# Kernel tuning notes

Hardware: AMD Instinct MI355X
Metric: run time of the kernel (lower is better)

## Reference

```python
import jax, jax.numpy as jnp
import numpy as np

N_NODES = 100000
N_EDGES = 600000
D = 128  # input_dim == output_dim (required by index_add into zeros_like(x) + residual)
EPS = 1e-5


def _linear_params(key, d_in, d_out):
    kw, kb = jax.random.split(key)
    bound = 1.0 / np.sqrt(d_in)
    w = jax.random.uniform(kw, (d_in, d_out), minval=-bound, maxval=bound, dtype=jnp.float32)
    b = jax.random.uniform(kb, (d_out,), minval=-bound, maxval=bound, dtype=jnp.float32)
    return w, b


def setup_inputs() -> dict:
    key = jax.random.key(0)
    ks = jax.random.split(key, 6)
    x = jax.random.normal(ks[0], (N_NODES, D), dtype=jnp.float32)
    edge_index = jax.random.randint(ks[1], (2, N_EDGES), 0, N_NODES, dtype=jnp.int32)
    w_m1, b_m1 = _linear_params(ks[2], 2 * D, D)
    w_m2, b_m2 = _linear_params(ks[3], D, D)
    w_u1, b_u1 = _linear_params(ks[4], 2 * D, D)
    w_u2, b_u2 = _linear_params(ks[5], D, D)
    gamma = jnp.ones((D,), dtype=jnp.float32)
    beta = jnp.zeros((D,), dtype=jnp.float32)
    return {
        "x": x, "edge_index": edge_index,
        "w_m1": w_m1, "b_m1": b_m1, "w_m2": w_m2, "b_m2": b_m2,
        "w_u1": w_u1, "b_u1": b_u1, "w_u2": w_u2, "b_u2": b_u2,
        "gamma": gamma, "beta": beta,
    }


def _layernorm(h, gamma, beta):
    mu = jnp.mean(h, axis=-1, keepdims=True)
    var = jnp.mean(jnp.square(h - mu), axis=-1, keepdims=True)
    return (h - mu) * jax.lax.rsqrt(var + EPS) * gamma + beta


def reference(x, edge_index, w_m1, b_m1, w_m2, b_m2, w_u1, b_u1, w_u2, b_u2, gamma, beta):
    row, col = edge_index[0], edge_index[1]
    # message MLP on concat of gathered endpoints: [E, 2D] -> [E, D]
    m_in = jnp.concatenate([x[row], x[col]], axis=-1)
    m = jax.nn.relu(m_in @ w_m1 + b_m1) @ w_m2 + b_m2
    # scatter-add messages to destination nodes (index_add along dim 0 with col)
    agg = jax.ops.segment_sum(m, col, num_segments=x.shape[0])
    # update MLP on [N, 2D] -> [N, D]
    u_in = jnp.concatenate([x, agg], axis=-1)
    h = jax.nn.relu(u_in @ w_u1 + b_u1) @ w_u2 + b_u2
    return _layernorm(h, gamma, beta) + x
```

## Files before the change

kernel.cpp:

```cpp
#include <hip/hip_runtime.h>
#include <hip/hip_bf16.h>
#include <stdint.h>

#define N_NODES 100000
#define N_EDGES 600000
#define D 128
#define EPS 1e-5f
#define SCAN_BS 512
#define ROW_MASK 0x1FFFF

#define PREP_BLOCKS 321
#define HIST_BLOCKS 2344
#define XF_BLOCKS   3125
#define SC_BLOCKS   2344
#define AGG_BLOCKS  12500
#define UPD_BLOCKS  3125

typedef __attribute__((ext_vector_type(8))) short short8;
typedef __attribute__((ext_vector_type(16))) float floatx16;


__device__ __forceinline__ uint32_t pack_bf16_rne(float lo, float hi) {
    uint32_t ul = __builtin_bit_cast(uint32_t, lo);
    uint32_t uh = __builtin_bit_cast(uint32_t, hi);
    ul += 0x7fffu + ((ul >> 16) & 1u);
    uh += 0x7fffu + ((uh >> 16) & 1u);
    return (ul >> 16) | (uh & 0xffff0000u);
}

__device__ __forceinline__ unsigned short f32_to_bf16_rne(float f) {
    uint32_t u = __builtin_bit_cast(uint32_t, f);
    u += 0x7fffu + ((u >> 16) & 1u);
    return (unsigned short)(u >> 16);
}

__device__ __forceinline__ float bflo(uint32_t a) { return __builtin_bit_cast(float, a << 16); }
__device__ __forceinline__ float bfhi(uint32_t a) { return __builtin_bit_cast(float, a & 0xffff0000u); }

__global__ void prep_hist(const float* __restrict__ w_m1, const float* __restrict__ w_u1,
                          const float* __restrict__ w_u2, const float* __restrict__ w_m2,
                          const float* __restrict__ b_m2,
                          unsigned short* __restrict__ wm1f, unsigned short* __restrict__ wu1tf,
                          unsigned short* __restrict__ wu2f, unsigned short* __restrict__ wcf,
                          float* __restrict__ vb,
                          const int* __restrict__ col, int* __restrict__ count,
                          int* __restrict__ rank) {
    if (blockIdx.x >= PREP_BLOCKS) {
        int e = (blockIdx.x - PREP_BLOCKS) * 256 + threadIdx.x;
        if (e < N_EDGES) rank[e] = atomicAdd(&count[col[e]], 1);
        return;
    }
    int idx = blockIdx.x * 256 + threadIdx.x;
    if (idx < 32768) {
        int j = idx & 7, lane = (idx >> 3) & 63, t = (idx >> 9) & 3, s = idx >> 11;
        int kk = s * 16 + ((lane >> 5) << 3) + j;
        wm1f[idx] = f32_to_bf16_rne(w_m1[kk * 128 + t * 32 + (lane & 31)]);
    } else if (idx < 49152) {
        int ii = idx - 32768;
        int j = ii & 7, lane = (ii >> 3) & 63, t = (ii >> 9) & 3, s = ii >> 11;
        int kk = s * 16 + ((lane >> 5) << 3) + j;
        wu1tf[ii] = f32_to_bf16_rne(w_u1[kk * 128 + t * 32 + (lane & 31)]);
    } else if (idx < 65536) {
        int ii = idx - 49152;
        int j = ii & 7, lane = (ii >> 3) & 63, t = (ii >> 9) & 3, s = ii >> 11;
        int kk = s * 16 + ((lane >> 5) << 3) + j;
        wu2f[ii] = f32_to_bf16_rne(w_u2[kk * 128 + t * 32 + (lane & 31)]);
    } else if (idx < 81920) {
        int ii = idx - 65536;
        int j = ii & 7, lane = (ii >> 3) & 63, t = (ii >> 9) & 3, s = ii >> 11;
        int kk = s * 16 + ((lane >> 5) << 3) + j;
        int nn = t * 32 + (lane & 31);
        float acc = 0.0f;
        for (int q = 0; q < 128; ++q)
            acc += w_m2[kk * 128 + q] * w_u1[(128 + q) * 128 + nn];
        wcf[ii] = f32_to_bf16_rne(acc);
    } else if (idx < 82048) {
        int nn = idx - 81920;
        float acc = 0.0f;
        for (int q = 0; q < 128; ++q)
            acc += b_m2[q] * w_u1[(128 + q) * 128 + nn];
        vb[nn] = acc;
    }
}

__global__ void scan_one(const int* __restrict__ count, int* __restrict__ base,
                         int* __restrict__ gcur) {
    __shared__ int tmp[SCAN_BS];
    __shared__ int bbase;
    int g = blockIdx.x * SCAN_BS + threadIdx.x;
    int v = (g < N_NODES) ? count[g] : 0;
    tmp[threadIdx.x] = v;
    __syncthreads();
    int acc = v;
#pragma unroll
    for (int off = 1; off < SCAN_BS; off <<= 1) {
        int add = (threadIdx.x >= off) ? tmp[threadIdx.x - off] : 0;
        __syncthreads();
        acc += add;
        tmp[threadIdx.x] = acc;
        __syncthreads();
    }
    if (threadIdx.x == SCAN_BS - 1) bbase = atomicAdd(gcur, acc);
    __syncthreads();
    if (g < N_NODES) base[g] = bbase + acc - v;
}

__launch_bounds__(64, 4)
__global__ void xform_scatter(const float* __restrict__ x, const short8* __restrict__ w1f,
                              const float* __restrict__ b1, unsigned short* __restrict__ xtb,
                              const int* __restrict__ row, const int* __restrict__ col,
                              const int* __restrict__ rank, const int* __restrict__ base,
                              int* __restrict__ srow) {
    if (blockIdx.x >= XF_BLOCKS) {
        int e4 = (((blockIdx.x - XF_BLOCKS) * 64 + threadIdx.x) << 2);
        if (e4 < N_EDGES) {
            int4 r4 = *(const int4*)(row + e4);
            int4 c4 = *(const int4*)(col + e4);
            int4 k4 = *(const int4*)(rank + e4);
            srow[base[c4.x] + k4.x] = r4.x | ((c4.x & 31) << 17);
            srow[base[c4.y] + k4.y] = r4.y | ((c4.y & 31) << 17);
            srow[base[c4.z] + k4.z] = r4.z | ((c4.z & 31) << 17);
            srow[base[c4.w] + k4.w] = r4.w | ((c4.w & 31) << 17);
        }
        return;
    }

    __shared__ __align__(16) short h1[32 * 136];
    const int lane = threadIdx.x;
    const int l31  = lane & 31;
    const int half = lane >> 5;
    short* hl = h1;

    const int nbase = blockIdx.x * 32;
    const int n = nbase + l31;
    const float* px = x + (size_t)n * D + half * 8;

    union { short8 v; uint32_t u[4]; } fa[8];
#pragma unroll
    for (int s = 0; s < 8; ++s) {
        const int off = s * 16;
        float4 a0 = *(const float4*)(px + off);
        float4 a1 = *(const float4*)(px + off + 4);
        fa[s].u[0] = pack_bf16_rne(a0.x, a0.y); fa[s].u[1] = pack_bf16_rne(a0.z, a0.w);
        fa[s].u[2] = pack_bf16_rne(a1.x, a1.y); fa[s].u[3] = pack_bf16_rne(a1.z, a1.w);
    }

#pragma unroll
    for (int p = 0; p < 2; ++p) {
        floatx16 acc[4];
#pragma unroll
        for (int t = 0; t < 4; ++t) acc[t] = (floatx16)0.0f;
#pragma unroll
        for (int s = 0; s < 8; ++s) {
#pragma unroll
            for (int t = 0; t < 4; ++t) {
                short8 wf = w1f[((p * 8 + s) * 4 + t) * 64 + lane];
                acc[t] = __builtin_amdgcn_mfma_f32_32x32x16_bf16(fa[s].v, wf, acc[t], 0, 0, 0);
            }
        }
#pragma unroll
        for (int t = 0; t < 4; ++t) {
            float bias = p ? b1[t * 32 + l31] : 0.0f;
#pragma unroll
            for (int r = 0; r < 16; ++r) {
                int m = (r & 3) + 8 * (r >> 2) + 4 * half;
                hl[m * 136 + t * 32 + l31] = (short)f32_to_bf16_rne(acc[t][r] + bias);
            }
        }
#pragma unroll
        for (int it = 0; it < 8; ++it) {
            int off = it * 512 + lane * 8;
            int r2 = off >> 7;
            int c2 = off & 127;
            short8 v = *(const short8*)(hl + r2 * 136 + c2);
            *(short8*)(xtb + (size_t)(nbase + r2) * 256 + p * 128 + c2) = v;
        }
    }
}

__launch_bounds__(64, 4)
__global__ void agg_kernel(uint32_t* __restrict__ xtb32, const int* __restrict__ srowpk,
                           const int* __restrict__ base, const int* __restrict__ count) {
    __shared__ __align__(16) uint32_t accu[8 * 64];
    __shared__ __align__(16) uint32_t XBl[8 * 64];
    const int lane = threadIdx.x;
    const int t    = lane & 15;
    const int q16  = lane & 48;

    const int nbase = blockIdx.x * 8;

    const int b_l = base[nbase + (lane & 7)];
    const int c_l = count[nbase + (lane & 7)];
    const int qsrc = q16 >> 3;
    const int qbeg = __shfl(b_l, qsrc);
    const int qend = __shfl(b_l, qsrc + 1) + __shfl(c_l, qsrc + 1);
    const int rembase = qend - qbeg;

    int ncm = (rembase + 7) >> 3;
    ncm = max(ncm, __shfl_xor(ncm, 16));
    ncm = max(ncm, __shfl_xor(ncm, 32));

    {
        uint4 z; z.x = 0; z.y = 0; z.z = 0; z.w = 0;
        *((uint4*)accu + lane) = z;
        *((uint4*)accu + 64 + lane) = z;
    }
#pragma unroll
    for (int it = 0; it < 2; ++it) {
        int fi4 = it * 64 + lane;
        int i = fi4 >> 4, k4 = fi4 & 15;
        *((uint4*)XBl + fi4) = *(const uint4*)(xtb32 + (size_t)(nbase + i) * 128 + 64 + (k4 << 2));
    }

    {
        float sl0 = 0.f, sl1 = 0.f, sl2 = 0.f, sl3 = 0.f;
        float sh0 = 0.f, sh1 = 0.f, sh2 = 0.f, sh3 = 0.f;
        int curnib = -1;

        auto flush = [&]() {
            uint4 o;
            o.x = pack_bf16_rne(sl0, sh0);
            o.y = pack_bf16_rne(sl1, sh1);
            o.z = pack_bf16_rne(sl2, sh2);
            o.w = pack_bf16_rne(sl3, sh3);
            *(uint4*)(accu + (curnib << 6) + (t << 2)) = o;
        };

        for (int c = 0; c < ncm; ++c) {
            int idx = qbeg + (c << 3) + (t & 7);
            int pk = srowpk[min(idx, N_EDGES - 1)];
            const int rem = rembase - (c << 3);

            uint4 xt[8]; int pv[8];
#pragma unroll
            for (int e = 0; e < 8; ++e) {
                int p = __shfl(pk, q16 + e);
                if (e >= rem) p = 0;
                pv[e] = p;
                xt[e] = *(const uint4*)(xtb32 + (size_t)(p & ROW_MASK) * 128 + (t << 2));
            }
            __builtin_amdgcn_sched_barrier(0);
#pragma unroll
            for (int e = 0; e < 8; ++e) {
                if (e < rem) {
                    int nib = (pv[e] >> 17) & 7;
                    uint4 xb = *(const uint4*)(XBl + (nib << 6) + (t << 2));
                    float a0 = fmaxf(bflo(xt[e].x) + bflo(xb.x), 0.f);
                    float b0 = fmaxf(bfhi(xt[e].x) + bfhi(xb.x), 0.f);
                    float a1 = fmaxf(bflo(xt[e].y) + bflo(xb.y), 0.f);
                    float b1 = fmaxf(bfhi(xt[e].y) + bfhi(xb.y), 0.f);
                    float a2 = fmaxf(bflo(xt[e].z) + bflo(xb.z), 0.f);
                    float b2 = fmaxf(bfhi(xt[e].z) + bfhi(xb.z), 0.f);
                    float a3 = fmaxf(bflo(xt[e].w) + bflo(xb.w), 0.f);
                    float b3 = fmaxf(bfhi(xt[e].w) + bfhi(xb.w), 0.f);
                    if (nib != curnib) {
                        if (curnib >= 0) flush();
                        curnib = nib;
                        sl0 = a0; sh0 = b0; sl1 = a1; sh1 = b1;
                        sl2 = a2; sh2 = b2; sl3 = a3; sh3 = b3;
                    } else {
                        sl0 += a0; sh0 += b0; sl1 += a1; sh1 += b1;
                        sl2 += a2; sh2 += b2; sl3 += a3; sh3 += b3;
                    }
                }
            }
        }
        if (curnib >= 0) flush();
    }

#pragma unroll
    for (int it = 0; it < 2; ++it) {
        int fi4 = it * 64 + lane;
        int i = fi4 >> 4, k4 = fi4 & 15;
        *(uint4*)(xtb32 + (size_t)(nbase + i) * 128 + 64 + (k4 << 2)) = *((uint4*)accu + fi4);
    }
}

__launch_bounds__(64, 4)
__global__ void upd_kernel(const float* __restrict__ x, const uint32_t* __restrict__ xtb32,
                           const int* __restrict__ count,
                           const short8* __restrict__ wu1tf, const short8* __restrict__ wcf,
                           const short8* __restrict__ wu2f,
                           const float* __restrict__ b_u1, const float* __restrict__ vb,
                           const float* __restrict__ b_u2,
                           const float* __restrict__ gamma, const float* __restrict__ beta,
                           float* __restrict__ out) {
    __shared__ __align__(16) short h1[32 * 136];
    const int lane = threadIdx.x;
    const int l31  = lane & 31;
    const int half = lane >> 5;
    short* hl = h1;

    const int nbase = blockIdx.x * 32;
    const int nc = nbase + l31;
    const float dgv = (float)count[nc];

    const float* px = x + (size_t)nc * D + half * 8;
    const short* xtbs = (const short*)xtb32;

    floatx16 acc[4];
#pragma unroll
    for (int tt = 0; tt < 4; ++tt) acc[tt] = (floatx16)0.0f;

#pragma unroll
    for (int s = 0; s < 16; ++s) {
        union { short8 v; uint32_t u[4]; } fa;
        const short8* bf;
        if (s < 8) {
            const int off = s * 16;
            float4 a0 = *(const float4*)(px + off);
            float4 a1 = *(const float4*)(px + off + 4);
            fa.u[0] = pack_bf16_rne(a0.x, a0.y); fa.u[1] = pack_bf16_rne(a0.z, a0.w);
            fa.u[2] = pack_bf16_rne(a1.x, a1.y); fa.u[3] = pack_bf16_rne(a1.z, a1.w);
            bf = wu1tf + (s * 4) * 64;
        } else {
            fa.v = *(const short8*)(xtbs + (size_t)nc * 256 + 128 + (s - 8) * 16 + half * 8);
            bf = wcf + ((s - 8) * 4) * 64;
        }
#pragma unroll
        for (int tt = 0; tt < 4; ++tt) {
            short8 wf = bf[tt * 64 + lane];
            acc[tt] = __builtin_amdgcn_mfma_f32_32x32x16_bf16(fa.v, wf, acc[tt], 0, 0, 0);
        }
    }

    float bu1[4], vbt[4];
#pragma unroll
    for (int tt = 0; tt < 4; ++tt) {
        bu1[tt] = b_u1[tt * 32 + l31];
        vbt[tt] = vb[tt * 32 + l31];
    }

#pragma unroll
    for (int r = 0; r < 16; ++r) {
        int m = (r & 3) + 8 * (r >> 2) + 4 * half;
        float dg = __shfl(dgv, m, 32);
#pragma unroll
        for (int tt = 0; tt < 4; ++tt) {
            float v = fmaxf(acc[tt][r] + bu1[tt] + dg * vbt[tt], 0.0f);
            hl[m * 136 + tt * 32 + l31] = (short)f32_to_bf16_rne(v);
        }
    }

    floatx16 acc2[4];
#pragma unroll
    for (int tt = 0; tt < 4; ++tt) acc2[tt] = (floatx16)0.0f;

#pragma unroll
    for (int s = 0; s < 8; ++s) {
        short8 af = *(const short8*)(hl + l31 * 136 + s * 16 + half * 8);
#pragma unroll
        for (int tt = 0; tt < 4; ++tt) {
            short8 wf = wu2f[(s * 4 + tt) * 64 + lane];
            acc2[tt] = __builtin_amdgcn_mfma_f32_32x32x16_bf16(af, wf, acc2[tt], 0, 0, 0);
        }
    }

    float g4[4], be4[4], bias2[4];
#pragma unroll
    for (int tt = 0; tt < 4; ++tt) {
        g4[tt]    = gamma[tt * 32 + l31];
        be4[tt]   = beta[tt * 32 + l31];
        bias2[tt] = b_u2[tt * 32 + l31];
    }

    float* hf = (float*)hl;
#pragma unroll
    for (int p = 0; p < 2; ++p) {
#pragma unroll
        for (int rr = 0; rr < 8; ++rr) {
            int r = p * 8 + rr;
            float hv[4];
            float s1 = 0.0f, s2 = 0.0f;
#pragma unroll
            for (int tt = 0; tt < 4; ++tt) {
                hv[tt] = acc2[tt][r] + bias2[tt];
                s1 += hv[tt];
                s2 += hv[tt] * hv[tt];
            }
#pragma unroll
            for (int mask = 1; mask < 32; mask <<= 1) {
                s1 += __shfl_xor(s1, mask);
                s2 += __shfl_xor(s2, mask);
            }
            float mean = s1 * (1.0f / 128.0f);
            float var  = s2 * (1.0f / 128.0f) - mean * mean;
            float rs   = rsqrtf(var + EPS);
            int m = (r & 3) + 8 * (r >> 2) + 4 * half;
            int mrow = m - 16 * p;
#pragma unroll
            for (int tt = 0; tt < 4; ++tt)
                hf[mrow * 132 + tt * 32 + l31] = (hv[tt] - mean) * rs * g4[tt] + be4[tt];
        }
#pragma unroll
        for (int it = 0; it < 8; ++it) {
            int qq = it * 64 + lane;
            int r2 = qq >> 5;
            int c4 = qq & 31;
            int node = nbase + 16 * p + r2;
            float4 v = *(const float4*)(hf + r2 * 132 + c4 * 4);
            float4 xr = *(const float4*)(x + (size_t)node * D + c4 * 4);
            v.x += xr.x; v.y += xr.y; v.z += xr.z; v.w += xr.w;
            *(float4*)(out + (size_t)node * D + c4 * 4) = v;
        }
    }
}

extern "C" void kernel_launch(void* const* d_in, const int* in_sizes, int n_in,
                              void* d_out, int out_size, void* d_ws, size_t ws_size,
                              hipStream_t stream) {
    const float* x     = (const float*)d_in[0];
    const int*   edge  = (const int*)d_in[1];
    const float* w_m1  = (const float*)d_in[2];
    const float* b_m1  = (const float*)d_in[3];
    const float* w_m2  = (const float*)d_in[4];
    const float* b_m2  = (const float*)d_in[5];
    const float* w_u1  = (const float*)d_in[6];
    const float* b_u1  = (const float*)d_in[7];
    const float* w_u2  = (const float*)d_in[8];
    const float* b_u2  = (const float*)d_in[9];
    const float* gamma = (const float*)d_in[10];
    const float* beta  = (const float*)d_in[11];
    float* out = (float*)d_out;

    char* ws = (char*)d_ws;
    size_t off = 0;
    auto alloc = [&](size_t bytes) { void* p = ws + off; off = (off + bytes + 15) & ~(size_t)15; return p; };

    unsigned short* xtb   = (unsigned short*)alloc((size_t)N_NODES * 256 * 2);
    unsigned short* wm1f  = (unsigned short*)alloc(256 * 128 * 2);
    unsigned short* wu1tf = (unsigned short*)alloc(128 * 128 * 2);
    unsigned short* wcf   = (unsigned short*)alloc(128 * 128 * 2);
    unsigned short* wu2f  = (unsigned short*)alloc(128 * 128 * 2);
    float* vb    = (float*)alloc(128 * 4);
    int* count   = (int*)alloc((size_t)N_NODES * 4 + 16);
    int* gcur    = count + N_NODES;
    int* base    = (int*)alloc((size_t)N_NODES * 4);
    int* rank    = (int*)alloc((size_t)N_EDGES * 4);
    int* srow    = (int*)alloc((size_t)N_EDGES * 4);

    const int* rowi = edge;
    const int* coli = edge + N_EDGES;
    const int NB = (N_NODES + SCAN_BS - 1) / SCAN_BS;

    (void)hipMemsetAsync(count, 0, (size_t)N_NODES * 4 + 16, stream);

    prep_hist<<<PREP_BLOCKS + HIST_BLOCKS, 256, 0, stream>>>(
        w_m1, w_u1, w_u2, w_m2, b_m2, wm1f, wu1tf, wu2f, wcf, vb, coli, count, rank);

    scan_one<<<NB, SCAN_BS, 0, stream>>>(count, base, gcur);

    xform_scatter<<<XF_BLOCKS + SC_BLOCKS, 64, 0, stream>>>(
        x, (const short8*)wm1f, b_m1, xtb, rowi, coli, rank, base, srow);

    agg_kernel<<<AGG_BLOCKS, 64, 0, stream>>>(
        (uint32_t*)xtb, srow, base, count);

    upd_kernel<<<UPD_BLOCKS, 64, 0, stream>>>(
        x, (const uint32_t*)xtb, count,
        (const short8*)wu1tf, (const short8*)wcf, (const short8*)wu2f,
        b_u1, vb, b_u2, gamma, beta, out);
}
```

Baseline: 257.1 us.

## Split transform blocks by output half and prefetch update-kernel operands

The node transform kernel now launches twice as many blocks, each computing one of the two 128-column output halves, which adds parallelism but loads and converts x twice. The update kernel preloads all A fragments up front and double-buffers weight fragments across output tiles, so memory latency can overlap the MFMA chains. Its launch bounds drop to 2 waves per SIMD, allowing more registers per thread at the cost of occupancy.

```diff
diff --git a/kernel.cpp b/kernel.cpp
--- a/kernel.cpp
+++ b/kernel.cpp
@@ -11,7 +11,7 @@
 
 #define PREP_BLOCKS 321
 #define HIST_BLOCKS 2344
-#define XF_BLOCKS   3125
+#define XF_BLOCKS   6250
 #define SC_BLOCKS   2344
 #define AGG_BLOCKS  12500
 #define UPD_BLOCKS  3125
@@ -131,7 +131,8 @@
     const int half = lane >> 5;
     short* hl = h1;
 
-    const int nbase = blockIdx.x * 32;
+    const int nbase = (blockIdx.x >> 1) * 32;
+    const int p     = blockIdx.x & 1;
     const int n = nbase + l31;
     const float* px = x + (size_t)n * D + half * 8;
 
@@ -145,36 +146,33 @@
         fa[s].u[2] = pack_bf16_rne(a1.x, a1.y); fa[s].u[3] = pack_bf16_rne(a1.z, a1.w);
     }
 
-#pragma unroll
-    for (int p = 0; p < 2; ++p) {
-        floatx16 acc[4];
-#pragma unroll
-        for (int t = 0; t < 4; ++t) acc[t] = (floatx16)0.0f;
-#pragma unroll
-        for (int s = 0; s < 8; ++s) {
-#pragma unroll
-            for (int t = 0; t < 4; ++t) {
-                short8 wf = w1f[((p * 8 + s) * 4 + t) * 64 + lane];
-                acc[t] = __builtin_amdgcn_mfma_f32_32x32x16_bf16(fa[s].v, wf, acc[t], 0, 0, 0);
-            }
-        }
+    floatx16 acc[4];
+#pragma unroll
+    for (int t = 0; t < 4; ++t) acc[t] = (floatx16)0.0f;
+#pragma unroll
+    for (int s = 0; s < 8; ++s) {
 #pragma unroll
         for (int t = 0; t < 4; ++t) {
-            float bias = p ? b1[t * 32 + l31] : 0.0f;
-#pragma unroll
-            for (int r = 0; r < 16; ++r) {
-                int m = (r & 3) + 8 * (r >> 2) + 4 * half;
-                hl[m * 136 + t * 32 + l31] = (short)f32_to_bf16_rne(acc[t][r] + bias);
-            }
-        }
-#pragma unroll
-        for (int it = 0; it < 8; ++it) {
-            int off = it * 512 + lane * 8;
-            int r2 = off >> 7;
-            int c2 = off & 127;
-            short8 v = *(const short8*)(hl + r2 * 136 + c2);
-            *(short8*)(xtb + (size_t)(nbase + r2) * 256 + p * 128 + c2) = v;
-        }
+            short8 wf = w1f[((p * 8 + s) * 4 + t) * 64 + lane];
+            acc[t] = __builtin_amdgcn_mfma_f32_32x32x16_bf16(fa[s].v, wf, acc[t], 0, 0, 0);
+        }
+    }
+#pragma unroll
+    for (int t = 0; t < 4; ++t) {
+        float bias = p ? b1[t * 32 + l31] : 0.0f;
+#pragma unroll
+        for (int r = 0; r < 16; ++r) {
+            int m = (r & 3) + 8 * (r >> 2) + 4 * half;
+            hl[m * 136 + t * 32 + l31] = (short)f32_to_bf16_rne(acc[t][r] + bias);
+        }
+    }
+#pragma unroll
+    for (int it = 0; it < 8; ++it) {
+        int off = it * 512 + lane * 8;
+        int r2 = off >> 7;
+        int c2 = off & 127;
+        short8 v = *(const short8*)(hl + r2 * 136 + c2);
+        *(short8*)(xtb + (size_t)(nbase + r2) * 256 + p * 128 + c2) = v;
     }
 }
 
@@ -276,7 +274,7 @@
     }
 }
 
-__launch_bounds__(64, 4)
+__launch_bounds__(64, 2)
 __global__ void upd_kernel(const float* __restrict__ x, const uint32_t* __restrict__ xtb32,
                            const int* __restrict__ count,
                            const short8* __restrict__ wu1tf, const short8* __restrict__ wcf,
@@ -298,29 +296,51 @@
     const float* px = x + (size_t)nc * D + half * 8;
     const short* xtbs = (const short*)xtb32;
 
+    short8 fa[16];
+    {
+        float4 xa[16];
+#pragma unroll
+        for (int s = 0; s < 8; ++s) {
+            xa[2 * s]     = *(const float4*)(px + s * 16);
+            xa[2 * s + 1] = *(const float4*)(px + s * 16 + 4);
+        }
+#pragma unroll
+        for (int s = 0; s < 8; ++s)
+            fa[8 + s] = *(const short8*)(xtbs + (size_t)nc * 256 + 128 + s * 16 + half * 8);
+#pragma unroll
+        for (int s = 0; s < 8; ++s) {
+            union { short8 v; uint32_t u[4]; } u;
+            u.u[0] = pack_bf16_rne(xa[2 * s].x, xa[2 * s].y);
+            u.u[1] = pack_bf16_rne(xa[2 * s].z, xa[2 * s].w);
+            u.u[2] = pack_bf16_rne(xa[2 * s + 1].x, xa[2 * s + 1].y);
+            u.u[3] = pack_bf16_rne(xa[2 * s + 1].z, xa[2 * s + 1].w);
+            fa[s] = u.v;
+        }
+    }
+
     floatx16 acc[4];
 #pragma unroll
     for (int tt = 0; tt < 4; ++tt) acc[tt] = (floatx16)0.0f;
 
-#pragma unroll
-    for (int s = 0; s < 16; ++s) {
-        union { short8 v; uint32_t u[4]; } fa;
-        const short8* bf;
-        if (s < 8) {
-            const int off = s * 16;
-            float4 a0 = *(const float4*)(px + off);
-            float4 a1 = *(const float4*)(px + off + 4);
-            fa.u[0] = pack_bf16_rne(a0.x, a0.y); fa.u[1] = pack_bf16_rne(a0.z, a0.w);
-            fa.u[2] = pack_bf16_rne(a1.x, a1.y); fa.u[3] = pack_bf16_rne(a1.z, a1.w);
-            bf = wu1tf + (s * 4) * 64;
-        } else {
-            fa.v = *(const short8*)(xtbs + (size_t)nc * 256 + 128 + (s - 8) * 16 + half * 8);
-            bf = wcf + ((s - 8) * 4) * 64;
-        }
-#pragma unroll
-        for (int tt = 0; tt < 4; ++tt) {
-            short8 wf = bf[tt * 64 + lane];
-            acc[tt] = __builtin_amdgcn_mfma_f32_32x32x16_bf16(fa.v, wf, acc[tt], 0, 0, 0);
+    {
+        short8 wfA[8], wfB[8];
+        auto ldw = [&](short8* dst, int stage) {
+            const int tt = stage >> 1;
+            const short8* m = (stage & 1) ? wcf : wu1tf;
+#pragma unroll
+            for (int j = 0; j < 8; ++j)
+                dst[j] = m[(j * 4 + tt) * 64 + lane];
+        };
+        ldw(wfA, 0);
+#pragma unroll
+        for (int k = 0; k < 8; ++k) {
+            short8* cur = (k & 1) ? wfB : wfA;
+            short8* nxt = (k & 1) ? wfA : wfB;
+            if (k < 7) ldw(nxt, k + 1);
+            const int tt = k >> 1, h = k & 1;
+#pragma unroll
+            for (int j = 0; j < 8; ++j)
+                acc[tt] = __builtin_amdgcn_mfma_f32_32x32x16_bf16(fa[h * 8 + j], cur[j], acc[tt], 0, 0, 0);
         }
     }
 
@@ -345,14 +365,27 @@
     floatx16 acc2[4];
 #pragma unroll
     for (int tt = 0; tt < 4; ++tt) acc2[tt] = (floatx16)0.0f;
-
-#pragma unroll
-    for (int s = 0; s < 8; ++s) {
-        short8 af = *(const short8*)(hl + l31 * 136 + s * 16 + half * 8);
+    {
+        short8 af[8];
+#pragma unroll
+        for (int s = 0; s < 8; ++s)
+            af[s] = *(const short8*)(hl + l31 * 136 + s * 16 + half * 8);
+
+        short8 vfA[8], vfB[8];
+        auto ldw2 = [&](short8* dst, int tt) {
+#pragma unroll
+            for (int j = 0; j < 8; ++j)
+                dst[j] = wu2f[(j * 4 + tt) * 64 + lane];
+        };
+        ldw2(vfA, 0);
 #pragma unroll
         for (int tt = 0; tt < 4; ++tt) {
-            short8 wf = wu2f[(s * 4 + tt) * 64 + lane];
-            acc2[tt] = __builtin_amdgcn_mfma_f32_32x32x16_bf16(af, wf, acc2[tt], 0, 0, 0);
+            short8* cur = (tt & 1) ? vfB : vfA;
+            short8* nxt = (tt & 1) ? vfA : vfB;
+            if (tt < 3) ldw2(nxt, tt + 1);
+#pragma unroll
+            for (int j = 0; j < 8; ++j)
+                acc2[tt] = __builtin_amdgcn_mfma_f32_32x32x16_bf16(af[j], cur[j], acc2[tt], 0, 0, 0);
         }
     }
 
```

Result: no change. 261.7 us (+1.8%).

## Fuse aggregation and update MLP into one 256-thread block kernel

Applied to the files above, without the earlier changes.

Merges the edge aggregation kernel and the node update kernel into a single kernel with four waves per block. Each block now handles 32 nodes, and each wave aggregates 8 of them. The aggregated bf16 features stay in LDS and feed the update MFMAs directly, so they are no longer written back to global memory and re-read, and one kernel launch is removed. The update GEMMs are split across the four waves by output column tile, which needs cross-wave LDS reductions for the layernorm statistics and several extra barriers. The packed destination index is now read with all its high bits instead of 3, so it assumes the scatter step encodes a 0-31 local node index.

```diff
diff --git a/kernel.cpp b/kernel.cpp
--- a/kernel.cpp
+++ b/kernel.cpp
@@ -13,8 +13,7 @@
 #define HIST_BLOCKS 2344
 #define XF_BLOCKS   3125
 #define SC_BLOCKS   2344
-#define AGG_BLOCKS  12500
-#define UPD_BLOCKS  3125
+#define AU_BLOCKS   3125
 
 typedef __attribute__((ext_vector_type(8))) short short8;
 typedef __attribute__((ext_vector_type(16))) float floatx16;
@@ -178,41 +177,58 @@
     }
 }
 
-__launch_bounds__(64, 4)
-__global__ void agg_kernel(uint32_t* __restrict__ xtb32, const int* __restrict__ srowpk,
-                           const int* __restrict__ base, const int* __restrict__ count) {
-    __shared__ __align__(16) uint32_t accu[8 * 64];
-    __shared__ __align__(16) uint32_t XBl[8 * 64];
-    const int lane = threadIdx.x;
+__launch_bounds__(256, 4)
+__global__ void aggupd_kernel(const float* __restrict__ x, const uint32_t* __restrict__ xtb32,
+                              const int* __restrict__ srowpk,
+                              const int* __restrict__ base, const int* __restrict__ count,
+                              const short8* __restrict__ wu1tf, const short8* __restrict__ wcf,
+                              const short8* __restrict__ wu2f,
+                              const float* __restrict__ b_u1, const float* __restrict__ vb,
+                              const float* __restrict__ b_u2,
+                              const float* __restrict__ gamma, const float* __restrict__ beta,
+                              float* __restrict__ out) {
+    __shared__ __align__(16) uint32_t accu[32 * 64];
+    __shared__ __align__(16) uint32_t XBl[32 * 64];
+    __shared__ __align__(16) short h1[32 * 136];
+    __shared__ float partS1[4][32], partS2[4][32];
+    __shared__ float meanA[32], rsA[32];
+
+    const int tid  = threadIdx.x;
+    const int wv   = tid >> 6;
+    const int lane = tid & 63;
+    const int l31  = lane & 31;
+    const int half = lane >> 5;
     const int t    = lane & 15;
     const int q16  = lane & 48;
 
-    const int nbase = blockIdx.x * 8;
-
-    const int b_l = base[nbase + (lane & 7)];
-    const int c_l = count[nbase + (lane & 7)];
-    const int qsrc = q16 >> 3;
-    const int qbeg = __shfl(b_l, qsrc);
-    const int qend = __shfl(b_l, qsrc + 1) + __shfl(c_l, qsrc + 1);
-    const int rembase = qend - qbeg;
-
-    int ncm = (rembase + 7) >> 3;
-    ncm = max(ncm, __shfl_xor(ncm, 16));
-    ncm = max(ncm, __shfl_xor(ncm, 32));
+    const int nbase = blockIdx.x * 32;
 
     {
         uint4 z; z.x = 0; z.y = 0; z.z = 0; z.w = 0;
-        *((uint4*)accu + lane) = z;
-        *((uint4*)accu + 64 + lane) = z;
-    }
-#pragma unroll
-    for (int it = 0; it < 2; ++it) {
-        int fi4 = it * 64 + lane;
-        int i = fi4 >> 4, k4 = fi4 & 15;
-        *((uint4*)XBl + fi4) = *(const uint4*)(xtb32 + (size_t)(nbase + i) * 128 + 64 + (k4 << 2));
-    }
+        *((uint4*)accu + tid) = z;
+        *((uint4*)accu + 256 + tid) = z;
+#pragma unroll
+        for (int it = 0; it < 2; ++it) {
+            int fi4 = it * 256 + tid;
+            int i = fi4 >> 4, k4 = fi4 & 15;
+            *((uint4*)XBl + fi4) = *(const uint4*)(xtb32 + (size_t)(nbase + i) * 128 + 64 + (k4 << 2));
+        }
+    }
+    __syncthreads();
 
     {
+        const int nodew = nbase + 8 * wv;
+        const int b_l = base[nodew + (lane & 7)];
+        const int c_l = count[nodew + (lane & 7)];
+        const int qsrc = q16 >> 3;
+        const int qbeg = __shfl(b_l, qsrc);
+        const int qend = __shfl(b_l, qsrc + 1) + __shfl(c_l, qsrc + 1);
+        const int rembase = qend - qbeg;
+
+        int ncm = (rembase + 7) >> 3;
+        ncm = max(ncm, __shfl_xor(ncm, 16));
+        ncm = max(ncm, __shfl_xor(ncm, 32));
+
         float sl0 = 0.f, sl1 = 0.f, sl2 = 0.f, sl3 = 0.f;
         float sh0 = 0.f, sh1 = 0.f, sh2 = 0.f, sh3 = 0.f;
         int curnib = -1;
@@ -243,7 +259,7 @@
 #pragma unroll
             for (int e = 0; e < 8; ++e) {
                 if (e < rem) {
-                    int nib = (pv[e] >> 17) & 7;
+                    int nib = pv[e] >> 17;
                     uint4 xb = *(const uint4*)(XBl + (nib << 6) + (t << 2));
                     float a0 = fmaxf(bflo(xt[e].x) + bflo(xb.x), 0.f);
                     float b0 = fmaxf(bfhi(xt[e].x) + bfhi(xb.x), 0.f);
@@ -267,142 +283,106 @@
         }
         if (curnib >= 0) flush();
     }
-
-#pragma unroll
-    for (int it = 0; it < 2; ++it) {
-        int fi4 = it * 64 + lane;
-        int i = fi4 >> 4, k4 = fi4 & 15;
-        *(uint4*)(xtb32 + (size_t)(nbase + i) * 128 + 64 + (k4 << 2)) = *((uint4*)accu + fi4);
-    }
-}
-
-__launch_bounds__(64, 4)
-__global__ void upd_kernel(const float* __restrict__ x, const uint32_t* __restrict__ xtb32,
-                           const int* __restrict__ count,
-                           const short8* __restrict__ wu1tf, const short8* __restrict__ wcf,
-                           const short8* __restrict__ wu2f,
-                           const float* __restrict__ b_u1, const float* __restrict__ vb,
-                           const float* __restrict__ b_u2,
-                           const float* __restrict__ gamma, const float* __restrict__ beta,
-                           float* __restrict__ out) {
-    __shared__ __align__(16) short h1[32 * 136];
-    const int lane = threadIdx.x;
-    const int l31  = lane & 31;
-    const int half = lane >> 5;
-    short* hl = h1;
-
-    const int nbase = blockIdx.x * 32;
+    __syncthreads();
+
     const int nc = nbase + l31;
     const float dgv = (float)count[nc];
-
     const float* px = x + (size_t)nc * D + half * 8;
-    const short* xtbs = (const short*)xtb32;
-
-    floatx16 acc[4];
-#pragma unroll
-    for (int tt = 0; tt < 4; ++tt) acc[tt] = (floatx16)0.0f;
-
-#pragma unroll
-    for (int s = 0; s < 16; ++s) {
+
+    const float bu1  = b_u1[wv * 32 + l31];
+    const float vbt  = vb[wv * 32 + l31];
+    const float bias2 = b_u2[wv * 32 + l31];
+    const float gA   = gamma[wv * 32 + l31];
+    const float beA  = beta[wv * 32 + l31];
+
+    floatx16 acc = (floatx16)0.0f;
+#pragma unroll
+    for (int s = 0; s < 8; ++s) {
         union { short8 v; uint32_t u[4]; } fa;
-        const short8* bf;
-        if (s < 8) {
-            const int off = s * 16;
-            float4 a0 = *(const float4*)(px + off);
-            float4 a1 = *(const float4*)(px + off + 4);
-            fa.u[0] = pack_bf16_rne(a0.x, a0.y); fa.u[1] = pack_bf16_rne(a0.z, a0.w);
-            fa.u[2] = pack_bf16_rne(a1.x, a1.y); fa.u[3] = pack_bf16_rne(a1.z, a1.w);
-            bf = wu1tf + (s * 4) * 64;
-        } else {
-            fa.v = *(const short8*)(xtbs + (size_t)nc * 256 + 128 + (s - 8) * 16 + half * 8);
-            bf = wcf + ((s - 8) * 4) * 64;
-        }
-#pragma unroll
-        for (int tt = 0; tt < 4; ++tt) {
-            short8 wf = bf[tt * 64 + lane];
-            acc[tt] = __builtin_amdgcn_mfma_f32_32x32x16_bf16(fa.v, wf, acc[tt], 0, 0, 0);
-        }
-    }
-
-    float bu1[4], vbt[4];
-#pragma unroll
-    for (int tt = 0; tt < 4; ++tt) {
-        bu1[tt] = b_u1[tt * 32 + l31];
-        vbt[tt] = vb[tt * 32 + l31];
+        const int off = s * 16;
+        float4 a0 = *(const float4*)(px + off);
+        float4 a1 = *(const float4*)(px + off + 4);
+        fa.u[0] = pack_bf16_rne(a0.x, a0.y); fa.u[1] = pack_bf16_rne(a0.z, a0.w);
+        fa.u[2] = pack_bf16_rne(a1.x, a1.y); fa.u[3] = pack_bf16_rne(a1.z, a1.w);
+        short8 wf = wu1tf[(s * 4 + wv) * 64 + lane];
+        acc = __builtin_amdgcn_mfma_f32_32x32x16_bf16(fa.v, wf, acc, 0, 0, 0);
+    }
+#pragma unroll
+    for (int s = 0; s < 8; ++s) {
+        short8 fh = *(const short8*)((const short*)accu + l31 * 128 + s * 16 + half * 8);
+        short8 wf = wcf[(s * 4 + wv) * 64 + lane];
+        acc = __builtin_amdgcn_mfma_f32_32x32x16_bf16(fh, wf, acc, 0, 0, 0);
     }
 
 #pragma unroll
     for (int r = 0; r < 16; ++r) {
         int m = (r & 3) + 8 * (r >> 2) + 4 * half;
         float dg = __shfl(dgv, m, 32);
-#pragma unroll
-        for (int tt = 0; tt < 4; ++tt) {
-            float v = fmaxf(acc[tt][r] + bu1[tt] + dg * vbt[tt], 0.0f);
-            hl[m * 136 + tt * 32 + l31] = (short)f32_to_bf16_rne(v);
-        }
-    }
-
-    floatx16 acc2[4];
-#pragma unroll
-    for (int tt = 0; tt < 4; ++tt) acc2[tt] = (floatx16)0.0f;
-
+        float v = fmaxf(acc[r] + bu1 + dg * vbt, 0.0f);
+        h1[m * 136 + wv * 32 + l31] = (short)f32_to_bf16_rne(v);
+    }
+    __syncthreads();
+
+    short8 af[8];
+#pragma unroll
+    for (int s = 0; s < 8; ++s)
+        af[s] = *(const short8*)(h1 + l31 * 136 + s * 16 + half * 8);
+    floatx16 acc2 = (floatx16)0.0f;
 #pragma unroll
     for (int s = 0; s < 8; ++s) {
-        short8 af = *(const short8*)(hl + l31 * 136 + s * 16 + half * 8);
-#pragma unroll
-        for (int tt = 0; tt < 4; ++tt) {
-            short8 wf = wu2f[(s * 4 + tt) * 64 + lane];
-            acc2[tt] = __builtin_amdgcn_mfma_f32_32x32x16_bf16(af, wf, acc2[tt], 0, 0, 0);
-        }
-    }
-
-    float g4[4], be4[4], bias2[4];
-#pragma unroll
-    for (int tt = 0; tt < 4; ++tt) {
-        g4[tt]    = gamma[tt * 32 + l31];
-        be4[tt]   = beta[tt * 32 + l31];
-        bias2[tt] = b_u2[tt * 32 + l31];
-    }
-
-    float* hf = (float*)hl;
+        short8 wf = wu2f[(s * 4 + wv) * 64 + lane];
+        acc2 = __builtin_amdgcn_mfma_f32_32x32x16_bf16(af[s], wf, acc2, 0, 0, 0);
+    }
+
+#pragma unroll
+    for (int r = 0; r < 16; ++r) {
+        float hv = acc2[r] + bias2;
+        float s1 = hv, s2 = hv * hv;
+#pragma unroll
+        for (int mask = 1; mask < 32; mask <<= 1) {
+            s1 += __shfl_xor(s1, mask);
+            s2 += __shfl_xor(s2, mask);
+        }
+        int m = (r & 3) + 8 * (r >> 2) + 4 * half;
+        if (l31 == 0) { partS1[wv][m] = s1; partS2[wv][m] = s2; }
+    }
+    __syncthreads();
+    if (tid < 32) {
+        int m = tid;
+        float s1 = partS1[0][m] + partS1[1][m] + partS1[2][m] + partS1[3][m];
+        float s2 = partS2[0][m] + partS2[1][m] + partS2[2][m] + partS2[3][m];
+        float mean = s1 * (1.0f / 128.0f);
+        float var  = s2 * (1.0f / 128.0f) - mean * mean;
+        meanA[m] = mean;
+        rsA[m]   = rsqrtf(var + EPS);
+    }
+    __syncthreads();
+
+    float* hf = (float*)h1;
 #pragma unroll
     for (int p = 0; p < 2; ++p) {
 #pragma unroll
-        for (int rr = 0; rr < 8; ++rr) {
-            int r = p * 8 + rr;
-            float hv[4];
-            float s1 = 0.0f, s2 = 0.0f;
-#pragma unroll
-            for (int tt = 0; tt < 4; ++tt) {
-                hv[tt] = acc2[tt][r] + bias2[tt];
-                s1 += hv[tt];
-                s2 += hv[tt] * hv[tt];
-            }
-#pragma unroll
-            for (int mask = 1; mask < 32; mask <<= 1) {
-                s1 += __shfl_xor(s1, mask);
-                s2 += __shfl_xor(s2, mask);
-            }
-            float mean = s1 * (1.0f / 128.0f);
-            float var  = s2 * (1.0f / 128.0f) - mean * mean;
-            float rs   = rsqrtf(var + EPS);
+        for (int r = 0; r < 16; ++r) {
             int m = (r & 3) + 8 * (r >> 2) + 4 * half;
             int mrow = m - 16 * p;
-#pragma unroll
-            for (int tt = 0; tt < 4; ++tt)
-                hf[mrow * 132 + tt * 32 + l31] = (hv[tt] - mean) * rs * g4[tt] + be4[tt];
-        }
-#pragma unroll
-        for (int it = 0; it < 8; ++it) {
-            int qq = it * 64 + lane;
-            int r2 = qq >> 5;
-            int c4 = qq & 31;
+            if (mrow >= 0 && mrow < 16) {
+                float hv = acc2[r] + bias2;
+                hf[mrow * 132 + wv * 32 + l31] = (hv - meanA[m]) * rsA[m] * gA + beA;
+            }
+        }
+        __syncthreads();
+#pragma unroll
+        for (int it = 0; it < 2; ++it) {
+            int q = it * 256 + tid;
+            int r2 = q >> 5;
+            int c4 = q & 31;
             int node = nbase + 16 * p + r2;
             float4 v = *(const float4*)(hf + r2 * 132 + c4 * 4);
             float4 xr = *(const float4*)(x + (size_t)node * D + c4 * 4);
             v.x += xr.x; v.y += xr.y; v.z += xr.z; v.w += xr.w;
             *(float4*)(out + (size_t)node * D + c4 * 4) = v;
         }
+        __syncthreads();
     }
 }
 
@@ -453,11 +433,8 @@
     xform_scatter<<<XF_BLOCKS + SC_BLOCKS, 64, 0, stream>>>(
         x, (const short8*)wm1f, b_m1, xtb, rowi, coli, rank, base, srow);
 
-    agg_kernel<<<AGG_BLOCKS, 64, 0, stream>>>(
-        (uint32_t*)xtb, srow, base, count);
-
-    upd_kernel<<<UPD_BLOCKS, 64, 0, stream>>>(
-        x, (const uint32_t*)xtb, count,
+    aggupd_kernel<<<AU_BLOCKS, 256, 0, stream>>>(
+        x, (const uint32_t*)xtb, srow, base, count,
         (const short8*)wu1tf, (const short8*)wcf, (const short8*)wu2f,
         b_u1, vb, b_u2, gamma, beta, out);
 }
```

Result: no change. 261.8 us (+1.8%).
